# Optimization experiments

Hardware: AMD Instinct MI355X
Metric: run time of the kernel (lower is better)

The kernel has to match this reference:

```python
import jax, jax.numpy as jnp
import numpy as np
import math

B, T, C = 4, 2048, 1024
NH, D = 16, 64  # n_head, head_dim; NH * D == C


def setup_inputs() -> dict:
    key = jax.random.key(0)
    ks = jax.random.split(key, 7)
    std = 0.02
    return {
        "x": jax.random.normal(ks[0], (B, T, C), dtype=jnp.float32),
        "W_attn": jax.random.normal(ks[1], (C, 3 * C), dtype=jnp.float32) * std,
        "b_attn": jax.random.normal(ks[2], (3 * C,), dtype=jnp.float32) * std,
        "bQ": jax.random.normal(ks[3], (NH, D), dtype=jnp.float32) * 0.1 + 0.5,
        "bK": jax.random.normal(ks[4], (NH, D), dtype=jnp.float32) * 0.1 + 0.3,
        "W_proj": jax.random.normal(ks[5], (C, C), dtype=jnp.float32) * std,
        "b_proj": jax.random.normal(ks[6], (C,), dtype=jnp.float32) * std,
    }


def reference(x, W_attn, b_attn, bQ, bK, W_proj, b_proj):
    Bx, Tx, Cx = x.shape
    qkv = x @ W_attn + b_attn                      # [B, T, 3C]
    q, k, v = jnp.split(qkv, 3, axis=2)
    # [B, T, C] -> [B, NH, T, D]
    q = q.reshape(Bx, Tx, NH, D).transpose(0, 2, 1, 3)
    k = k.reshape(Bx, Tx, NH, D).transpose(0, 2, 1, 3)
    v = v.reshape(Bx, Tx, NH, D).transpose(0, 2, 1, 3)
    # per-head disorder bias added to Q and K before the dot product
    q = q + bQ[None, :, None, :]
    k = k + bK[None, :, None, :]
    scores = jnp.einsum('bhqd,bhkd->bhqk', q, k) / math.sqrt(D)  # [B, NH, T, T]
    causal = jnp.tril(jnp.ones((Tx, Tx), dtype=bool))
    scores = jnp.where(causal[None, None], scores, jnp.float32(-jnp.inf))
    att = jax.nn.softmax(scores, axis=-1)
    y = jnp.einsum('bhqk,bhkd->bhqd', att, v)      # [B, NH, T, D]
    y = y.transpose(0, 2, 1, 3).reshape(Bx, Tx, Cx)
    return y @ W_proj + b_proj
```

## Files before the change

kernel.cpp:

```cpp
#include <hip/hip_runtime.h>

typedef unsigned short u16;
typedef unsigned int u32;
typedef __bf16 bf16x8 __attribute__((ext_vector_type(8)));
typedef float f32x4 __attribute__((ext_vector_type(4)));

#define B_  4
#define T_  2048
#define C_  1024
#define NH_ 16
#define D_  64
#define M_  (B_*T_)
#define N_QKV (3*C_)

#define ATTN_BLOCKS 1024

#define BARRIER()  __asm__ __volatile__("s_barrier" ::: "memory")
#define WAIT_VM4() __asm__ __volatile__("s_waitcnt vmcnt(4)" ::: "memory")
#define WAIT_VM0() __asm__ __volatile__("s_waitcnt vmcnt(0)" ::: "memory")

__device__ __forceinline__ void async_copy16(void* lds, const void* gptr) {
  __builtin_amdgcn_global_load_lds(
      (const __attribute__((address_space(1))) u32*)gptr,
      (__attribute__((address_space(3))) u32*)(u32)(uintptr_t)lds,
      16, 0, 0);
}

__device__ __forceinline__ u16 f2bf(float f) {
  union { float f; unsigned u; } c; c.f = f;
  unsigned u = c.u;
  unsigned r = (u + 0x7fffu + ((u >> 16) & 1u)) >> 16;
  return (u16)r;
}

__global__ __launch_bounds__(256) void conv_bf16(const float* __restrict__ in,
                                                 u16* __restrict__ out, int n) {
  int i = (blockIdx.x * 256 + threadIdx.x) * 4;
  if (i < n) {
    float4 f = *reinterpret_cast<const float4*>(in + i);
    u16 o[4] = { f2bf(f.x), f2bf(f.y), f2bf(f.z), f2bf(f.w) };
    *reinterpret_cast<uint2*>(out + i) = *reinterpret_cast<uint2*>(o);
  }
}

__global__ __launch_bounds__(256) void transpose_bf16(const float* __restrict__ in,
                                                      u16* __restrict__ out,
                                                      int K, int N) {
  __shared__ float tile[32][33];
  int bi = blockIdx.y;
  int bj = blockIdx.x;
  int tx = threadIdx.x & 31;
  int ty = threadIdx.x >> 5;
#pragma unroll
  for (int i = 0; i < 4; ++i) {
    int row = ty + i * 8;
    tile[row][tx] = in[(bi * 32 + row) * N + bj * 32 + tx];
  }
  __syncthreads();
#pragma unroll
  for (int i = 0; i < 4; ++i) {
    int row = ty + i * 8;
    out[(bj * 32 + row) * K + bi * 32 + tx] = f2bf(tile[tx][row]);
  }
}

__global__ __launch_bounds__(256) void gemm_qkv(const u16* __restrict__ A,
                                                const u16* __restrict__ Bt,
                                                const float* __restrict__ b_attn,
                                                const float* __restrict__ bQ,
                                                const float* __restrict__ bK,
                                                u16* __restrict__ qo,
                                                u16* __restrict__ ko,
                                                u16* __restrict__ vo) {
  const int K = C_;
  int bm = blockIdx.y, bn = blockIdx.x;
  int tid = threadIdx.x;
  int wid = tid >> 6, lane = tid & 63;
  int lm = lane & 15, lq = lane >> 4;
  int wm = (wid >> 1) * 64, wn = (wid & 1) * 64;

  __shared__ u16 As[128 * 32];
  __shared__ u16 Bs[128 * 32];

  f32x4 acc[4][4];
#pragma unroll
  for (int i = 0; i < 4; ++i)
#pragma unroll
    for (int j = 0; j < 4; ++j) acc[i][j] = (f32x4){0.f, 0.f, 0.f, 0.f};

  const u16* Ab = A + (bm * 128) * K;
  const u16* Bb = Bt + (bn * 128) * K;
  int srow = lane >> 2;
  int scol = (lane & 3) * 8;

  for (int k0 = 0; k0 < K; k0 += 32) {
    __syncthreads();
#pragma unroll
    for (int j = 0; j < 2; ++j) {
      int c = wid * 2 + j;
      int row = c * 16 + srow;
      async_copy16(&As[c * 512], Ab + row * K + k0 + scol);
      async_copy16(&Bs[c * 512], Bb + row * K + k0 + scol);
    }
    __syncthreads();
    bf16x8 af[4], bf[4];
#pragma unroll
    for (int mt = 0; mt < 4; ++mt)
      af[mt] = *reinterpret_cast<const bf16x8*>(&As[(wm + mt * 16 + lm) * 32 + lq * 8]);
#pragma unroll
    for (int nt = 0; nt < 4; ++nt)
      bf[nt] = *reinterpret_cast<const bf16x8*>(&Bs[(wn + nt * 16 + lm) * 32 + lq * 8]);
#pragma unroll
    for (int mt = 0; mt < 4; ++mt)
#pragma unroll
      for (int nt = 0; nt < 4; ++nt)
        acc[mt][nt] = __builtin_amdgcn_mfma_f32_16x16x32_bf16(af[mt], bf[nt], acc[mt][nt], 0, 0, 0);
  }

  const float qscale = 0.18033688011112042f;
#pragma unroll
  for (int mt = 0; mt < 4; ++mt) {
#pragma unroll
    for (int nt = 0; nt < 4; ++nt) {
#pragma unroll
      for (int r = 0; r < 4; ++r) {
        int m = bm * 128 + wm + mt * 16 + lq * 4 + r;
        int n = bn * 128 + wn + nt * 16 + lm;
        float val = acc[mt][nt][r] + b_attn[n];
        int sel = n >> 10;
        int c = n & 1023;
        int h = c >> 6;
        int d = c & 63;
        int b = m >> 11;
        int t = m & 2047;
        if (sel == 0)      qo[(((b * NH_ + h) * T_) + t) * D_ + d] = f2bf((val + bQ[c]) * qscale);
        else if (sel == 1) ko[(((b * NH_ + h) * T_) + t) * D_ + d] = f2bf(val + bK[c]);
        else               vo[(((b * NH_ + h) * D_) + d) * T_ + t] = f2bf(val);
      }
    }
  }
}

__global__ __launch_bounds__(256, 4) void attn_kernel(const u16* __restrict__ q,
                                                      const u16* __restrict__ k,
                                                      const u16* __restrict__ vt,
                                                      u16* __restrict__ y) {
  int tid = threadIdx.x;
  int w = tid >> 6, lane = tid & 63;
  int lm = lane & 15, lq = lane >> 4;

  __shared__ u16 Ks[2][64 * 64];
  __shared__ u16 Vs[2][64 * 64];

  int srow = lane >> 3;
  int sg   = (lane & 7) ^ srow;

  int idx = blockIdx.x;
  int c8 = idx & 255, jq = idx >> 8;
  int a = c8 & 7, gq = c8 >> 3;
  int qt, bh;
  if (jq == 0)      { qt = 15 - a; bh = gq; }
  else if (jq == 1) { qt = 8 + a;  bh = 32 + gq; }
  else if (jq == 2) { qt = 7 - a;  bh = gq; }
  else              { qt = a;      bh = 32 + gq; }

  int b = bh >> 4, h = bh & 15;
  const int klast = 2 * qt + 1;
  const int qrow0 = qt * 128 + w * 32;

  const u16* qb = q + ((size_t)bh * T_ + qrow0) * D_;
  const u16* kb = k + (size_t)bh * T_ * D_;
  const u16* vb = vt + (size_t)bh * D_ * T_;

  auto stage_K = [&](int buf, int kbi) {
    const u16* gb = kb + (size_t)(kbi * 64) * 64;
#pragma unroll
    for (int j = 0; j < 2; ++j) {
      int c = w * 2 + j;
      async_copy16(&Ks[buf][c * 512], gb + (c * 8 + srow) * 64 + sg * 8);
    }
  };
  auto stage_V = [&](int buf, int kbi) {
    const u16* gb = vb + kbi * 64;
#pragma unroll
    for (int j = 0; j < 2; ++j) {
      int c = w * 2 + j;
      async_copy16(&Vs[buf][c * 512], gb + (size_t)(c * 8 + srow) * T_ + sg * 8);
    }
  };

  bf16x8 bq[2][2];
#pragma unroll
  for (int qt2 = 0; qt2 < 2; ++qt2) {
    const u16* qp = qb + (qt2 * 16 + lm) * D_ + lq * 8;
    bq[qt2][0] = *reinterpret_cast<const bf16x8*>(qp);
    bq[qt2][1] = *reinterpret_cast<const bf16x8*>(qp + 32);
  }

  f32x4 o[4][2];
#pragma unroll
  for (int dt = 0; dt < 4; ++dt)
#pragma unroll
    for (int qt2 = 0; qt2 < 2; ++qt2) o[dt][qt2] = (f32x4){0.f, 0.f, 0.f, 0.f};
  float mprev[2] = {-1e30f, -1e30f}, lsum[2] = {0.f, 0.f};

  stage_K(0, 0); stage_V(0, 0);
  stage_K(1, 1); stage_V(1, 1);

  for (int kbi = 0; kbi <= klast; ++kbi) {
    int buf = kbi & 1;
    WAIT_VM4();
    BARRIER();

    bf16x8 kf[4][2];
#pragma unroll
    for (int kt = 0; kt < 4; ++kt) {
      const u16* base = &Ks[buf][(kt * 16 + lm) * 64];
      kf[kt][0] = *reinterpret_cast<const bf16x8*>(base + ((lq ^ (lm & 7)) * 8));
      kf[kt][1] = *reinterpret_cast<const bf16x8*>(base + (((4 + lq) ^ (lm & 7)) * 8));
    }

    f32x4 s[4][2];
#pragma unroll
    for (int kt = 0; kt < 4; ++kt)
#pragma unroll
      for (int qt2 = 0; qt2 < 2; ++qt2) {
        f32x4 z = (f32x4){0.f, 0.f, 0.f, 0.f};
        z = __builtin_amdgcn_mfma_f32_16x16x32_bf16(kf[kt][0], bq[qt2][0], z, 0, 0, 0);
        z = __builtin_amdgcn_mfma_f32_16x16x32_bf16(kf[kt][1], bq[qt2][1], z, 0, 0, 0);
        s[kt][qt2] = z;
      }

    bool maskt = (kbi * 64 + 63 > qrow0);
    bf16x8 pb[2][2];
#pragma unroll
    for (int qt2 = 0; qt2 < 2; ++qt2) {
      int qg = qrow0 + qt2 * 16 + lm;
      if (maskt) {
#pragma unroll
        for (int kt = 0; kt < 4; ++kt)
#pragma unroll
          for (int r = 0; r < 4; ++r) {
            int key = kbi * 64 + kt * 16 + lq * 4 + r;
            if (key > qg) s[kt][qt2][r] = -1e30f;
          }
      }
      float mx[4];
#pragma unroll
      for (int kt = 0; kt < 4; ++kt)
        mx[kt] = fmaxf(fmaxf(s[kt][qt2][0], s[kt][qt2][1]),
                       fmaxf(s[kt][qt2][2], s[kt][qt2][3]));
      float mval = fmaxf(fmaxf(mx[0], mx[1]), fmaxf(mx[2], mx[3]));
      mval = fmaxf(mval, __shfl_xor(mval, 16));
      mval = fmaxf(mval, __shfl_xor(mval, 32));
      float mold = mprev[qt2];
      float mnew = fmaxf(mold, mval);
      unsigned long long upd = __ballot(mval > mold);
      if (upd) {
        float alpha = __builtin_exp2f(mold - mnew);
        lsum[qt2] *= alpha;
#pragma unroll
        for (int dt = 0; dt < 4; ++dt) o[dt][qt2] *= alpha;
        mprev[qt2] = mnew;
      }
      float rs = 0.f;
      unsigned pw[8];
#pragma unroll
      for (int kt = 0; kt < 4; ++kt) {
        unsigned pu[4];
#pragma unroll
        for (int r = 0; r < 4; ++r) {
          float p = __builtin_exp2f(s[kt][qt2][r] - mnew);
          rs += p;
          union { float f; unsigned u; } cc; cc.f = p;
          pu[r] = cc.u;
        }
        pw[kt * 2]     = __builtin_amdgcn_perm(pu[1], pu[0], 0x07060302u);
        pw[kt * 2 + 1] = __builtin_amdgcn_perm(pu[3], pu[2], 0x07060302u);
      }
      rs += __shfl_xor(rs, 16);
      rs += __shfl_xor(rs, 32);
      lsum[qt2] += rs;
      union { unsigned u[4]; bf16x8 v; } b0, b1;
#pragma unroll
      for (int t = 0; t < 4; ++t) { b0.u[t] = pw[t]; b1.u[t] = pw[4 + t]; }
      pb[qt2][0] = b0.v;
      pb[qt2][1] = b1.v;
    }

    {
      int r7 = lm & 7;
      int h4 = (lq & 1) * 4;
      int g0 = lq >> 1;
#pragma unroll
      for (int dt = 0; dt < 4; ++dt) {
        const u16* vbase = &Vs[buf][(dt * 16 + lm) * 64];
        union { unsigned long long qd[2]; bf16x8 v; } t0, t1;
        t0.qd[0] = *reinterpret_cast<const unsigned long long*>(vbase + ((g0 ^ r7) * 8) + h4);
        t0.qd[1] = *reinterpret_cast<const unsigned long long*>(vbase + (((g0 + 2) ^ r7) * 8) + h4);
        t1.qd[0] = *reinterpret_cast<const unsigned long long*>(vbase + (((g0 + 4) ^ r7) * 8) + h4);
        t1.qd[1] = *reinterpret_cast<const unsigned long long*>(vbase + (((g0 + 6) ^ r7) * 8) + h4);
#pragma unroll
        for (int qt2 = 0; qt2 < 2; ++qt2) {
          o[dt][qt2] = __builtin_amdgcn_mfma_f32_16x16x32_bf16(t0.v, pb[qt2][0], o[dt][qt2], 0, 0, 0);
          o[dt][qt2] = __builtin_amdgcn_mfma_f32_16x16x32_bf16(t1.v, pb[qt2][1], o[dt][qt2], 0, 0, 0);
        }
      }
    }

    BARRIER();
    int nk = (kbi + 2 <= klast) ? kbi + 2 : klast;
    stage_K(buf, nk); stage_V(buf, nk);
  }

  WAIT_VM0();

#pragma unroll
  for (int qt2 = 0; qt2 < 2; ++qt2) {
    float inv = 1.f / lsum[qt2];
    int qg = qrow0 + qt2 * 16 + lm;
#pragma unroll
    for (int dt = 0; dt < 4; ++dt) {
      u16 wb[4];
#pragma unroll
      for (int r = 0; r < 4; ++r) wb[r] = f2bf(o[dt][qt2][r] * inv);
      int d = dt * 16 + lq * 4;
      *reinterpret_cast<uint2*>(&y[((size_t)(b * T_ + qg) * NH_ + h) * D_ + d]) =
          *reinterpret_cast<uint2*>(wb);
    }
  }
}

__global__ __launch_bounds__(256) void gemm_proj(const u16* __restrict__ A,
                                                 const u16* __restrict__ Bt,
                                                 const float* __restrict__ b_proj,
                                                 float* __restrict__ out) {
  const int K = C_, N = C_;
  int bm = blockIdx.y, bn = blockIdx.x;
  int tid = threadIdx.x;
  int wid = tid >> 6, lane = tid & 63;
  int lm = lane & 15, lq = lane >> 4;
  int wm = (wid >> 1) * 64, wn = (wid & 1) * 64;

  __shared__ u16 As[128 * 32];
  __shared__ u16 Bs[128 * 32];

  f32x4 acc[4][4];
#pragma unroll
  for (int i = 0; i < 4; ++i)
#pragma unroll
    for (int j = 0; j < 4; ++j) acc[i][j] = (f32x4){0.f, 0.f, 0.f, 0.f};

  const u16* Ab = A + (bm * 128) * K;
  const u16* Bb = Bt + (bn * 128) * K;
  int srow = lane >> 2;
  int scol = (lane & 3) * 8;

  for (int k0 = 0; k0 < K; k0 += 32) {
    __syncthreads();
#pragma unroll
    for (int j = 0; j < 2; ++j) {
      int c = wid * 2 + j;
      int row = c * 16 + srow;
      async_copy16(&As[c * 512], Ab + row * K + k0 + scol);
      async_copy16(&Bs[c * 512], Bb + row * K + k0 + scol);
    }
    __syncthreads();
    bf16x8 af[4], bf[4];
#pragma unroll
    for (int mt = 0; mt < 4; ++mt)
      af[mt] = *reinterpret_cast<const bf16x8*>(&As[(wm + mt * 16 + lm) * 32 + lq * 8]);
#pragma unroll
    for (int nt = 0; nt < 4; ++nt)
      bf[nt] = *reinterpret_cast<const bf16x8*>(&Bs[(wn + nt * 16 + lm) * 32 + lq * 8]);
#pragma unroll
    for (int mt = 0; mt < 4; ++mt)
#pragma unroll
      for (int nt = 0; nt < 4; ++nt)
        acc[mt][nt] = __builtin_amdgcn_mfma_f32_16x16x32_bf16(af[mt], bf[nt], acc[mt][nt], 0, 0, 0);
  }

#pragma unroll
  for (int mt = 0; mt < 4; ++mt) {
#pragma unroll
    for (int nt = 0; nt < 4; ++nt) {
#pragma unroll
      for (int r = 0; r < 4; ++r) {
        int m = bm * 128 + wm + mt * 16 + lq * 4 + r;
        int n = bn * 128 + wn + nt * 16 + lm;
        out[m * N + n] = acc[mt][nt][r] + b_proj[n];
      }
    }
  }
}

extern "C" void kernel_launch(void* const* d_in, const int* in_sizes, int n_in,
                              void* d_out, int out_size, void* d_ws, size_t ws_size,
                              hipStream_t stream) {
  const float* x      = (const float*)d_in[0];
  const float* W_attn = (const float*)d_in[1];
  const float* b_attn = (const float*)d_in[2];
  const float* bQ     = (const float*)d_in[3];
  const float* bK     = (const float*)d_in[4];
  const float* W_proj = (const float*)d_in[5];
  const float* b_proj = (const float*)d_in[6];
  float* out = (float*)d_out;

  char* ws = (char*)d_ws;
  u16* xb  = (u16*)(ws);
  u16* WaT = (u16*)(ws + 16777216);
  u16* WpT = (u16*)(ws + 23068672);
  u16* qw  = (u16*)(ws + 25165824);
  u16* kw  = (u16*)(ws + 41943040);
  u16* vw  = (u16*)(ws + 58720256);
  u16* yw  = (u16*)(ws + 75497472);

  conv_bf16<<<M_ * C_ / (4 * 256), 256, 0, stream>>>(x, xb, M_ * C_);
  {
    dim3 g(N_QKV / 32, C_ / 32);
    transpose_bf16<<<g, 256, 0, stream>>>(W_attn, WaT, C_, N_QKV);
  }
  {
    dim3 g(C_ / 32, C_ / 32);
    transpose_bf16<<<g, 256, 0, stream>>>(W_proj, WpT, C_, C_);
  }
  {
    dim3 g(N_QKV / 128, M_ / 128);
    gemm_qkv<<<g, 256, 0, stream>>>(xb, WaT, b_attn, bQ, bK, qw, kw, vw);
  }
  attn_kernel<<<ATTN_BLOCKS, 256, 0, stream>>>(qw, kw, vw, yw);
  {
    dim3 g(C_ / 128, M_ / 128);
    gemm_proj<<<g, 256, 0, stream>>>(yw, WpT, b_proj, out);
  }
}
```

Before: 317.0 us.

## Double-buffer GEMMs with swizzled LDS, remap blocks, and fold softmax sum into MFMA

Both GEMMs now stage 64-wide K tiles into double-buffered, XOR-swizzled LDS, so global loads overlap the MFMAs and the per-iteration barriers drop. Blocks are remapped from a 1D grid with an XCD-aware interleave, and the kernels get a two-block occupancy hint. In attention, the row sum is computed by an extra MFMA against a ones row appended to V, which replaces the shuffle reductions. Rescaling is now lazy and only happens when the max grows by more than 8, which adds LDS usage and some risk of exponent growth in exchange for fewer rescales.

```diff
diff --git a/kernel.cpp b/kernel.cpp
--- a/kernel.cpp
+++ b/kernel.cpp
@@ -2,6 +2,7 @@
 
 typedef unsigned short u16;
 typedef unsigned int u32;
+typedef unsigned long long u64;
 typedef __bf16 bf16x8 __attribute__((ext_vector_type(8)));
 typedef float f32x4 __attribute__((ext_vector_type(4)));
 
@@ -17,7 +18,9 @@
 
 #define BARRIER()  __asm__ __volatile__("s_barrier" ::: "memory")
 #define WAIT_VM4() __asm__ __volatile__("s_waitcnt vmcnt(4)" ::: "memory")
+#define WAIT_VM8() __asm__ __volatile__("s_waitcnt vmcnt(8)" ::: "memory")
 #define WAIT_VM0() __asm__ __volatile__("s_waitcnt vmcnt(0)" ::: "memory")
+#define LGKM0()    __asm__ __volatile__("s_waitcnt lgkmcnt(0)" ::: "memory")
 
 __device__ __forceinline__ void async_copy16(void* lds, const void* gptr) {
   __builtin_amdgcn_global_load_lds(
@@ -64,23 +67,26 @@
   }
 }
 
-__global__ __launch_bounds__(256) void gemm_qkv(const u16* __restrict__ A,
-                                                const u16* __restrict__ Bt,
-                                                const float* __restrict__ b_attn,
-                                                const float* __restrict__ bQ,
-                                                const float* __restrict__ bK,
-                                                u16* __restrict__ qo,
-                                                u16* __restrict__ ko,
-                                                u16* __restrict__ vo) {
+__global__ __launch_bounds__(256, 2) void gemm_qkv(const u16* __restrict__ A,
+                                                   const u16* __restrict__ Bt,
+                                                   const float* __restrict__ b_attn,
+                                                   const float* __restrict__ bQ,
+                                                   const float* __restrict__ bK,
+                                                   u16* __restrict__ qo,
+                                                   u16* __restrict__ ko,
+                                                   u16* __restrict__ vo) {
   const int K = C_;
-  int bm = blockIdx.y, bn = blockIdx.x;
+  int bid = blockIdx.x;
+  int wg = (bid & 7) * 192 + (bid >> 3);
+  int bm = wg / 24, bn = wg % 24;
+
   int tid = threadIdx.x;
   int wid = tid >> 6, lane = tid & 63;
   int lm = lane & 15, lq = lane >> 4;
   int wm = (wid >> 1) * 64, wn = (wid & 1) * 64;
 
-  __shared__ u16 As[128 * 32];
-  __shared__ u16 Bs[128 * 32];
+  __shared__ u16 As[2][128 * 64];
+  __shared__ u16 Bs[2][128 * 64];
 
   f32x4 acc[4][4];
 #pragma unroll
@@ -88,34 +94,55 @@
 #pragma unroll
     for (int j = 0; j < 4; ++j) acc[i][j] = (f32x4){0.f, 0.f, 0.f, 0.f};
 
-  const u16* Ab = A + (bm * 128) * K;
-  const u16* Bb = Bt + (bn * 128) * K;
-  int srow = lane >> 2;
-  int scol = (lane & 3) * 8;
-
-  for (int k0 = 0; k0 < K; k0 += 32) {
-    __syncthreads();
-#pragma unroll
-    for (int j = 0; j < 2; ++j) {
-      int c = wid * 2 + j;
-      int row = c * 16 + srow;
-      async_copy16(&As[c * 512], Ab + row * K + k0 + scol);
-      async_copy16(&Bs[c * 512], Bb + row * K + k0 + scol);
-    }
-    __syncthreads();
-    bf16x8 af[4], bf[4];
+  const u16* Ab = A + (size_t)(bm * 128) * K;
+  const u16* Bb = Bt + (size_t)(bn * 128) * K;
+  int srow = lane >> 3;
+  int sgc  = ((lane & 7) ^ srow) * 8;
+
+  auto stage = [&](int bb, int t) {
+#pragma unroll
+    for (int i = 0; i < 4; ++i) {
+      int c = i * 4 + wid;
+      async_copy16(&As[bb][c * 512], Ab + (size_t)(c * 8 + srow) * K + t * 64 + sgc);
+      async_copy16(&Bs[bb][c * 512], Bb + (size_t)(c * 8 + srow) * K + t * 64 + sgc);
+    }
+  };
+
+  stage(0, 0);
+  const int NT = K / 64;
+  for (int t = 0; t < NT; ++t) {
+    int bb = t & 1;
+    int tn = (t + 1 < NT) ? t + 1 : t;
+    stage(bb ^ 1, tn);
+    WAIT_VM8();
+    BARRIER();
+    bf16x8 af[4][2], bf[4][2];
+#pragma unroll
+    for (int mt = 0; mt < 4; ++mt) {
+      const u16* base = &As[bb][(wm + mt * 16 + lm) * 64];
+#pragma unroll
+      for (int kh = 0; kh < 2; ++kh)
+        af[mt][kh] = *reinterpret_cast<const bf16x8*>(base + (((kh * 4 + lq) ^ (lm & 7)) * 8));
+    }
+#pragma unroll
+    for (int nt = 0; nt < 4; ++nt) {
+      const u16* base = &Bs[bb][(wn + nt * 16 + lm) * 64];
+#pragma unroll
+      for (int kh = 0; kh < 2; ++kh)
+        bf[nt][kh] = *reinterpret_cast<const bf16x8*>(base + (((kh * 4 + lq) ^ (lm & 7)) * 8));
+    }
 #pragma unroll
     for (int mt = 0; mt < 4; ++mt)
-      af[mt] = *reinterpret_cast<const bf16x8*>(&As[(wm + mt * 16 + lm) * 32 + lq * 8]);
-#pragma unroll
-    for (int nt = 0; nt < 4; ++nt)
-      bf[nt] = *reinterpret_cast<const bf16x8*>(&Bs[(wn + nt * 16 + lm) * 32 + lq * 8]);
-#pragma unroll
-    for (int mt = 0; mt < 4; ++mt)
 #pragma unroll
       for (int nt = 0; nt < 4; ++nt)
-        acc[mt][nt] = __builtin_amdgcn_mfma_f32_16x16x32_bf16(af[mt], bf[nt], acc[mt][nt], 0, 0, 0);
-  }
+#pragma unroll
+        for (int kh = 0; kh < 2; ++kh)
+          acc[mt][nt] = __builtin_amdgcn_mfma_f32_16x16x32_bf16(af[mt][kh], bf[nt][kh],
+                                                                acc[mt][nt], 0, 0, 0);
+    LGKM0();
+    BARRIER();
+  }
+  WAIT_VM0();
 
   const float qscale = 0.18033688011112042f;
 #pragma unroll
@@ -133,9 +160,9 @@
         int d = c & 63;
         int b = m >> 11;
         int t = m & 2047;
-        if (sel == 0)      qo[(((b * NH_ + h) * T_) + t) * D_ + d] = f2bf((val + bQ[c]) * qscale);
-        else if (sel == 1) ko[(((b * NH_ + h) * T_) + t) * D_ + d] = f2bf(val + bK[c]);
-        else               vo[(((b * NH_ + h) * D_) + d) * T_ + t] = f2bf(val);
+        if (sel == 0)      qo[(((size_t)(b * NH_ + h) * T_) + t) * D_ + d] = f2bf((val + bQ[c]) * qscale);
+        else if (sel == 1) ko[(((size_t)(b * NH_ + h) * T_) + t) * D_ + d] = f2bf(val + bK[c]);
+        else               vo[(((size_t)(b * NH_ + h) * D_) + d) * T_ + t] = f2bf(val);
       }
     }
   }
@@ -150,10 +177,18 @@
   int lm = lane & 15, lq = lane >> 4;
 
   __shared__ u16 Ks[2][64 * 64];
-  __shared__ u16 Vs[2][64 * 64];
+  __shared__ u16 Vs[2][80 * 64];
 
   int srow = lane >> 3;
   int sg   = (lane & 7) ^ srow;
+
+  for (int i = tid; i < 2 * 16 * 64; i += 256) {
+    int bufi = i >> 10;
+    int r = (i >> 6) & 15;
+    int c = i & 63;
+    Vs[bufi][(64 + r) * 64 + c] = (r == 0) ? (u16)0x3F80 : (u16)0;
+  }
+  __syncthreads();
 
   int idx = blockIdx.x;
   int c8 = idx & 255, jq = idx >> 8;
@@ -197,12 +232,14 @@
     bq[qt2][1] = *reinterpret_cast<const bf16x8*>(qp + 32);
   }
 
-  f32x4 o[4][2];
+  f32x4 o[4][2], o5[2];
 #pragma unroll
   for (int dt = 0; dt < 4; ++dt)
 #pragma unroll
     for (int qt2 = 0; qt2 < 2; ++qt2) o[dt][qt2] = (f32x4){0.f, 0.f, 0.f, 0.f};
-  float mprev[2] = {-1e30f, -1e30f}, lsum[2] = {0.f, 0.f};
+  o5[0] = (f32x4){0.f, 0.f, 0.f, 0.f};
+  o5[1] = (f32x4){0.f, 0.f, 0.f, 0.f};
+  float mprev[2] = {-1e30f, -1e30f};
 
   stage_K(0, 0); stage_V(0, 0);
   stage_K(1, 1); stage_V(1, 1);
@@ -254,33 +291,28 @@
       mval = fmaxf(mval, __shfl_xor(mval, 16));
       mval = fmaxf(mval, __shfl_xor(mval, 32));
       float mold = mprev[qt2];
-      float mnew = fmaxf(mold, mval);
-      unsigned long long upd = __ballot(mval > mold);
-      if (upd) {
+      if (__ballot(mval > mold + 8.f)) {
+        float mnew = fmaxf(mold, mval);
         float alpha = __builtin_exp2f(mold - mnew);
-        lsum[qt2] *= alpha;
 #pragma unroll
         for (int dt = 0; dt < 4; ++dt) o[dt][qt2] *= alpha;
+        o5[qt2] *= alpha;
         mprev[qt2] = mnew;
       }
-      float rs = 0.f;
+      float m = mprev[qt2];
       unsigned pw[8];
 #pragma unroll
       for (int kt = 0; kt < 4; ++kt) {
         unsigned pu[4];
 #pragma unroll
         for (int r = 0; r < 4; ++r) {
-          float p = __builtin_exp2f(s[kt][qt2][r] - mnew);
-          rs += p;
+          float p = __builtin_exp2f(s[kt][qt2][r] - m);
           union { float f; unsigned u; } cc; cc.f = p;
           pu[r] = cc.u;
         }
         pw[kt * 2]     = __builtin_amdgcn_perm(pu[1], pu[0], 0x07060302u);
         pw[kt * 2 + 1] = __builtin_amdgcn_perm(pu[3], pu[2], 0x07060302u);
       }
-      rs += __shfl_xor(rs, 16);
-      rs += __shfl_xor(rs, 32);
-      lsum[qt2] += rs;
       union { unsigned u[4]; bf16x8 v; } b0, b1;
 #pragma unroll
       for (int t = 0; t < 4; ++t) { b0.u[t] = pw[t]; b1.u[t] = pw[4 + t]; }
@@ -292,20 +324,35 @@
       int r7 = lm & 7;
       int h4 = (lq & 1) * 4;
       int g0 = lq >> 1;
+      bf16x8 v5[2];
+      {
+        const u16* vb5 = &Vs[buf][(64 + lm) * 64];
+        union { u64 qd[2]; bf16x8 v; } t0, t1;
+        t0.qd[0] = *reinterpret_cast<const u64*>(vb5 + ((g0 ^ r7) * 8) + h4);
+        t0.qd[1] = *reinterpret_cast<const u64*>(vb5 + (((g0 + 2) ^ r7) * 8) + h4);
+        t1.qd[0] = *reinterpret_cast<const u64*>(vb5 + (((g0 + 4) ^ r7) * 8) + h4);
+        t1.qd[1] = *reinterpret_cast<const u64*>(vb5 + (((g0 + 6) ^ r7) * 8) + h4);
+        v5[0] = t0.v; v5[1] = t1.v;
+      }
 #pragma unroll
       for (int dt = 0; dt < 4; ++dt) {
         const u16* vbase = &Vs[buf][(dt * 16 + lm) * 64];
-        union { unsigned long long qd[2]; bf16x8 v; } t0, t1;
-        t0.qd[0] = *reinterpret_cast<const unsigned long long*>(vbase + ((g0 ^ r7) * 8) + h4);
-        t0.qd[1] = *reinterpret_cast<const unsigned long long*>(vbase + (((g0 + 2) ^ r7) * 8) + h4);
-        t1.qd[0] = *reinterpret_cast<const unsigned long long*>(vbase + (((g0 + 4) ^ r7) * 8) + h4);
-        t1.qd[1] = *reinterpret_cast<const unsigned long long*>(vbase + (((g0 + 6) ^ r7) * 8) + h4);
+        union { u64 qd[2]; bf16x8 v; } t0, t1;
+        t0.qd[0] = *reinterpret_cast<const u64*>(vbase + ((g0 ^ r7) * 8) + h4);
+        t0.qd[1] = *reinterpret_cast<const u64*>(vbase + (((g0 + 2) ^ r7) * 8) + h4);
+        t1.qd[0] = *reinterpret_cast<const u64*>(vbase + (((g0 + 4) ^ r7) * 8) + h4);
+        t1.qd[1] = *reinterpret_cast<const u64*>(vbase + (((g0 + 6) ^ r7) * 8) + h4);
 #pragma unroll
         for (int qt2 = 0; qt2 < 2; ++qt2) {
           o[dt][qt2] = __builtin_amdgcn_mfma_f32_16x16x32_bf16(t0.v, pb[qt2][0], o[dt][qt2], 0, 0, 0);
           o[dt][qt2] = __builtin_amdgcn_mfma_f32_16x16x32_bf16(t1.v, pb[qt2][1], o[dt][qt2], 0, 0, 0);
         }
       }
+#pragma unroll
+      for (int qt2 = 0; qt2 < 2; ++qt2) {
+        o5[qt2] = __builtin_amdgcn_mfma_f32_16x16x32_bf16(v5[0], pb[qt2][0], o5[qt2], 0, 0, 0);
+        o5[qt2] = __builtin_amdgcn_mfma_f32_16x16x32_bf16(v5[1], pb[qt2][1], o5[qt2], 0, 0, 0);
+      }
     }
 
     BARRIER();
@@ -317,7 +364,8 @@
 
 #pragma unroll
   for (int qt2 = 0; qt2 < 2; ++qt2) {
-    float inv = 1.f / lsum[qt2];
+    float ls = __shfl(o5[qt2][0], lm);
+    float inv = 1.f / ls;
     int qg = qrow0 + qt2 * 16 + lm;
 #pragma unroll
     for (int dt = 0; dt < 4; ++dt) {
@@ -331,19 +379,22 @@
   }
 }
 
-__global__ __launch_bounds__(256) void gemm_proj(const u16* __restrict__ A,
-                                                 const u16* __restrict__ Bt,
-                                                 const float* __restrict__ b_proj,
-                                                 float* __restrict__ out) {
+__global__ __launch_bounds__(256, 2) void gemm_proj(const u16* __restrict__ A,
+                                                    const u16* __restrict__ Bt,
+                                                    const float* __restrict__ b_proj,
+                                                    float* __restrict__ out) {
   const int K = C_, N = C_;
-  int bm = blockIdx.y, bn = blockIdx.x;
+  int bid = blockIdx.x;
+  int wg = (bid & 7) * 64 + (bid >> 3);
+  int bm = wg / 8, bn = wg % 8;
+
   int tid = threadIdx.x;
   int wid = tid >> 6, lane = tid & 63;
   int lm = lane & 15, lq = lane >> 4;
   int wm = (wid >> 1) * 64, wn = (wid & 1) * 64;
 
-  __shared__ u16 As[128 * 32];
-  __shared__ u16 Bs[128 * 32];
+  __shared__ u16 As[2][128 * 64];
+  __shared__ u16 Bs[2][128 * 64];
 
   f32x4 acc[4][4];
 #pragma unroll
@@ -351,34 +402,55 @@
 #pragma unroll
     for (int j = 0; j < 4; ++j) acc[i][j] = (f32x4){0.f, 0.f, 0.f, 0.f};
 
-  const u16* Ab = A + (bm * 128) * K;
-  const u16* Bb = Bt + (bn * 128) * K;
-  int srow = lane >> 2;
-  int scol = (lane & 3) * 8;
-
-  for (int k0 = 0; k0 < K; k0 += 32) {
-    __syncthreads();
-#pragma unroll
-    for (int j = 0; j < 2; ++j) {
-      int c = wid * 2 + j;
-      int row = c * 16 + srow;
-      async_copy16(&As[c * 512], Ab + row * K + k0 + scol);
-      async_copy16(&Bs[c * 512], Bb + row * K + k0 + scol);
-    }
-    __syncthreads();
-    bf16x8 af[4], bf[4];
+  const u16* Ab = A + (size_t)(bm * 128) * K;
+  const u16* Bb = Bt + (size_t)(bn * 128) * K;
+  int srow = lane >> 3;
+  int sgc  = ((lane & 7) ^ srow) * 8;
+
+  auto stage = [&](int bb, int t) {
+#pragma unroll
+    for (int i = 0; i < 4; ++i) {
+      int c = i * 4 + wid;
+      async_copy16(&As[bb][c * 512], Ab + (size_t)(c * 8 + srow) * K + t * 64 + sgc);
+      async_copy16(&Bs[bb][c * 512], Bb + (size_t)(c * 8 + srow) * K + t * 64 + sgc);
+    }
+  };
+
+  stage(0, 0);
+  const int NT = K / 64;
+  for (int t = 0; t < NT; ++t) {
+    int bb = t & 1;
+    int tn = (t + 1 < NT) ? t + 1 : t;
+    stage(bb ^ 1, tn);
+    WAIT_VM8();
+    BARRIER();
+    bf16x8 af[4][2], bf[4][2];
+#pragma unroll
+    for (int mt = 0; mt < 4; ++mt) {
+      const u16* base = &As[bb][(wm + mt * 16 + lm) * 64];
+#pragma unroll
+      for (int kh = 0; kh < 2; ++kh)
+        af[mt][kh] = *reinterpret_cast<const bf16x8*>(base + (((kh * 4 + lq) ^ (lm & 7)) * 8));
+    }
+#pragma unroll
+    for (int nt = 0; nt < 4; ++nt) {
+      const u16* base = &Bs[bb][(wn + nt * 16 + lm) * 64];
+#pragma unroll
+      for (int kh = 0; kh < 2; ++kh)
+        bf[nt][kh] = *reinterpret_cast<const bf16x8*>(base + (((kh * 4 + lq) ^ (lm & 7)) * 8));
+    }
 #pragma unroll
     for (int mt = 0; mt < 4; ++mt)
-      af[mt] = *reinterpret_cast<const bf16x8*>(&As[(wm + mt * 16 + lm) * 32 + lq * 8]);
-#pragma unroll
-    for (int nt = 0; nt < 4; ++nt)
-      bf[nt] = *reinterpret_cast<const bf16x8*>(&Bs[(wn + nt * 16 + lm) * 32 + lq * 8]);
-#pragma unroll
-    for (int mt = 0; mt < 4; ++mt)
 #pragma unroll
       for (int nt = 0; nt < 4; ++nt)
-        acc[mt][nt] = __builtin_amdgcn_mfma_f32_16x16x32_bf16(af[mt], bf[nt], acc[mt][nt], 0, 0, 0);
-  }
+#pragma unroll
+        for (int kh = 0; kh < 2; ++kh)
+          acc[mt][nt] = __builtin_amdgcn_mfma_f32_16x16x32_bf16(af[mt][kh], bf[nt][kh],
+                                                                acc[mt][nt], 0, 0, 0);
+    LGKM0();
+    BARRIER();
+  }
+  WAIT_VM0();
 
 #pragma unroll
   for (int mt = 0; mt < 4; ++mt) {
@@ -388,7 +460,7 @@
       for (int r = 0; r < 4; ++r) {
         int m = bm * 128 + wm + mt * 16 + lq * 4 + r;
         int n = bn * 128 + wn + nt * 16 + lm;
-        out[m * N + n] = acc[mt][nt][r] + b_proj[n];
+        out[(size_t)m * N + n] = acc[mt][nt][r] + b_proj[n];
       }
     }
   }
@@ -424,13 +496,7 @@
     dim3 g(C_ / 32, C_ / 32);
     transpose_bf16<<<g, 256, 0, stream>>>(W_proj, WpT, C_, C_);
   }
-  {
-    dim3 g(N_QKV / 128, M_ / 128);
-    gemm_qkv<<<g, 256, 0, stream>>>(xb, WaT, b_attn, bQ, bK, qw, kw, vw);
-  }
+  gemm_qkv<<<(M_ / 128) * (N_QKV / 128), 256, 0, stream>>>(xb, WaT, b_attn, bQ, bK, qw, kw, vw);
   attn_kernel<<<ATTN_BLOCKS, 256, 0, stream>>>(qw, kw, vw, yw);
-  {
-    dim3 g(C_ / 128, M_ / 128);
-    gemm_proj<<<g, 256, 0, stream>>>(yw, WpT, b_proj, out);
-  }
-}
+  gemm_proj<<<(M_ / 128) * (C_ / 128), 256, 0, stream>>>(yw, WpT, b_proj, out);
+}
```

Result: slower. 337.8 us (+6.6%).
